# Performance work log

Measured on AMD Instinct MI355X. Metric: run time of the kernel, lower is better.

The kernel has to match this reference:

```python
import jax, jax.numpy as jnp
import numpy as np

KSIZE = 51  # radius=50 is even -> incremented to 51 in __init__


def _gaussian_1d(ksize):
    # cv2.getGaussianKernel with sigma<=0: sigma = 0.3*((ksize-1)*0.5 - 1) + 0.8
    sigma = 0.3 * ((ksize - 1) * 0.5 - 1) + 0.8
    x = np.arange(ksize, dtype=np.float64) - (ksize - 1) / 2
    g = np.exp(-(x * x) / (2.0 * sigma * sigma))
    g = g / g.sum()
    return g.astype(np.float32)


def _blur(img, kernel1d):
    """Separable Gaussian blur with reflect padding.
    Mathematically identical to the 2D conv with outer(g, g) in the torch code.
    img: (b, c, h, w), kernel1d: (k,)
    """
    k = kernel1d.shape[0]
    p = k // 2
    b, c, h, w = img.shape
    x = jnp.pad(img, ((0, 0), (0, 0), (p, p), (p, p)), mode='reflect')
    x = x.reshape(b * c, 1, h + 2 * p, w + 2 * p)
    # vertical pass then horizontal pass (conv vs correlation irrelevant: symmetric kernel)
    kv = kernel1d.reshape(1, 1, k, 1)
    kh = kernel1d.reshape(1, 1, 1, k)
    dn = ('NCHW', 'OIHW', 'NCHW')
    x = jax.lax.conv_general_dilated(x, kv, (1, 1), 'VALID', dimension_numbers=dn)
    x = jax.lax.conv_general_dilated(x, kh, (1, 1), 'VALID', dimension_numbers=dn)
    return x.reshape(b, c, h, w)


def setup_inputs() -> dict:
    key = jax.random.key(0)
    img = jax.random.uniform(key, (16, 3, 512, 512), dtype=jnp.float32)
    kernel1d = jnp.asarray(_gaussian_1d(KSIZE))
    return {"img": img, "kernel1d": kernel1d}


def reference(img, kernel1d):
    weight = 0.5
    threshold = 10.0
    blur = _blur(img, kernel1d)
    residual = img - blur
    mask = (jnp.abs(residual) * 255.0 > threshold).astype(img.dtype)
    soft_mask = _blur(mask, kernel1d)
    sharp = jnp.clip(img + weight * residual, 0.0, 1.0)
    return soft_mask * sharp + (1.0 - soft_mask) * img
```

## Files before the change

### kernel.cpp

```cpp
#include <hip/hip_runtime.h>
#include <hip/hip_bf16.h>


typedef __attribute__((ext_vector_type(8))) short bf16x8;
typedef __attribute__((ext_vector_type(4))) float f32x4;

constexpr int IMG = 512, NIMG = 48, K = 51;
constexpr int SP = 136;
constexpr int YP = 136;
constexpr int SROWS = 128;
constexpr int SDATA = 122;

__device__ __forceinline__ float bf2f(unsigned short u) {
    return __builtin_bit_cast(float, (unsigned)u << 16);
}
__device__ __forceinline__ unsigned short f2bf(float f) {
    unsigned u = __builtin_bit_cast(unsigned, f);
    u += 0x7FFF + ((u >> 16) & 1);
    return (unsigned short)(u >> 16);
}
__device__ __forceinline__ int refl(int i) {
    i = i < 0 ? -i : i;
    return i >= IMG ? 2 * IMG - 2 - i : i;
}

template <int PASS>
__global__ __launch_bounds__(512, 6) void usm_kern(const float* __restrict__ img,
                                                   unsigned short* __restrict__ resbuf,
                                                   unsigned char* __restrict__ maskbuf,
                                                   float* __restrict__ out,
                                                   const float* __restrict__ k1d) {
    __shared__ unsigned short st[SROWS * SP];
    __shared__ unsigned short Hl[64 * YP];

    const int tid = threadIdx.x, lane = tid & 63;
    const int wv = __builtin_amdgcn_readfirstlane(tid >> 6);
    const int m16 = lane & 15, g = lane >> 4;

    const int id = blockIdx.x;
    const int sw = (id & 7) * 384 + (id >> 3);
    const int bz = sw >> 6, r6 = sw & 63, byy = r6 >> 3, bxx = r6 & 7;
    const int x0 = bxx * 64, y0 = byy * 64;
    const size_t base = (size_t)bz * (IMG * IMG);
    const float* __restrict__ imgb = img + base;
    unsigned short* __restrict__ resb = resbuf + base;
    unsigned char* __restrict__ maskb = maskbuf + base;
    float* __restrict__ outb = out + base;

    bf16x8 a_v[2], a_h[2];
#pragma unroll
    for (int rs = 0; rs < 2; ++rs) {
        float gt[9];
#pragma unroll
        for (int e = 0; e < 9; ++e) {
            const int t = 32 * rs + 8 * g + e - m16;
            gt[e] = ((unsigned)t < (unsigned)K) ? k1d[t] : 0.f;
        }
#pragma unroll
        for (int j = 0; j < 8; ++j) {
            a_v[rs][j] = (short)f2bf(gt[j]);
            a_h[rs][j] = (short)f2bf(gt[j + 1]);
        }
    }
    const float gg0 = k1d[0], gg49 = k1d[49], gg50 = k1d[50];

    const bool xedge = (bxx == 0) | (bxx == 7);
    const int r0t = tid >> 4, c8 = (tid & 15) * 8;
#pragma unroll
    for (int j = 0; j < 4; ++j) {
        const int s = r0t + 32 * j;
        const int rowo = refl(y0 - 33 + min(s, SDATA - 1)) * IMG + (x0 - 32 + c8);
        unsigned pk[4];
        if (PASS == 0) {
            float v[8];
            if (!xedge) {
                const f32x4 f0 = *(const f32x4*)&imgb[rowo];
                const f32x4 f1 = *(const f32x4*)&imgb[rowo + 4];
#pragma unroll
                for (int e = 0; e < 4; ++e) { v[e] = f0[e]; v[e + 4] = f1[e]; }
            } else {
                const int rb = rowo - (x0 - 32 + c8);
#pragma unroll
                for (int e = 0; e < 8; ++e) v[e] = imgb[rb + refl(x0 - 32 + c8 + e)];
            }
#pragma unroll
            for (int w = 0; w < 4; ++w)
                pk[w] = (unsigned)f2bf(v[2 * w]) | ((unsigned)f2bf(v[2 * w + 1]) << 16);
        } else {
            unsigned char mb[8];
            if (!xedge) {
                const uint2 mv = *(const uint2*)&maskb[rowo];
#pragma unroll
                for (int e = 0; e < 4; ++e) {
                    mb[e] = (unsigned char)(mv.x >> (8 * e));
                    mb[e + 4] = (unsigned char)(mv.y >> (8 * e));
                }
            } else {
                const int rb = rowo - (x0 - 32 + c8);
#pragma unroll
                for (int e = 0; e < 8; ++e) mb[e] = maskb[rb + refl(x0 - 32 + c8 + e)];
            }
#pragma unroll
            for (int w = 0; w < 4; ++w)
                pk[w] = (mb[2 * w] ? 0x3F80u : 0u) | ((mb[2 * w + 1] ? 0x3F80u : 0u) << 16);
        }
        *(uint4*)&st[s * SP + c8] = make_uint4(pk[0], pk[1], pk[2], pk[3]);
    }
    __syncthreads();

#pragma unroll
    for (int k4 = 0; k4 < 4; ++k4) {
        const int t = wv + 8 * k4;
        const int xs = t & 3, yt = t >> 2;
        const int n = 16 * yt + m16;
        f32x4 acc = {0.f, 0.f, 0.f, 0.f};
#pragma unroll
        for (int rs = 0; rs < 2; ++rs) {
            const bf16x8 b = *(const bf16x8*)&st[n * SP + 16 * xs + 8 + 32 * rs + 8 * g];
            acc = __builtin_amdgcn_mfma_f32_16x16x32_bf16(a_h[rs], b, acc, 0, 0, 0);
        }
        if (g == 0) acc[0] = fmaf(gg0,  bf2f(st[n * SP + 16 * xs + 7]),  acc[0]);
        if (g == 3) acc[3] = fmaf(gg50, bf2f(st[n * SP + 16 * xs + 72]), acc[3]);
#pragma unroll
        for (int q = 0; q < 4; ++q)
            Hl[(16 * xs + 4 * g + q) * YP + n] = f2bf(acc[q]);
    }
    __syncthreads();

#pragma unroll
    for (int k2 = 0; k2 < 2; ++k2) {
        const int t = wv + 8 * k2;
        const int xs2 = t & 3, ys = t >> 2;
        const int xl = 16 * xs2 + m16;
        f32x4 acc = {0.f, 0.f, 0.f, 0.f};
#pragma unroll
        for (int rs = 0; rs < 2; ++rs) {
            const bf16x8 b = *(const bf16x8*)&Hl[xl * YP + 16 * ys + 8 + 32 * rs + 8 * g];
            acc = __builtin_amdgcn_mfma_f32_16x16x32_bf16(a_v[rs], b, acc, 0, 0, 0);
        }
        if (g == 3) {
            const float h72 = bf2f(Hl[xl * YP + 16 * ys + 72]);
            const float h73 = bf2f(Hl[xl * YP + 16 * ys + 73]);
            acc[2] = fmaf(gg50, h72, acc[2]);
            acc[3] = fmaf(gg49, h72, fmaf(gg50, h73, acc[3]));
        }
        const int yl0 = 16 * ys + 4 * g;
#pragma unroll
        for (int q = 0; q < 4; ++q) {
            const int di = (y0 + yl0 + q) * IMG + (x0 + xl);
            const float iv = imgb[di];
            if (PASS == 0) {
                const float rv = iv - acc[q];
                resb[di] = f2bf(rv);
                maskb[di] = (fabsf(rv) * 255.0f > 10.0f) ? 1 : 0;
            } else {
                const float rv = bf2f(resb[di]);
                float sharp = fmaf(0.5f, rv, iv);
                sharp = fminf(fmaxf(sharp, 0.f), 1.f);
                outb[di] = fmaf(acc[q], sharp - iv, iv);
            }
        }
    }
}

extern "C" void kernel_launch(void* const* d_in, const int* in_sizes, int n_in,
                              void* d_out, int out_size, void* d_ws, size_t ws_size,
                              hipStream_t stream) {
    (void)in_sizes; (void)n_in; (void)out_size; (void)ws_size;
    const float* img = (const float*)d_in[0];
    const float* k1d = (const float*)d_in[1];
    float* out = (float*)d_out;
    unsigned short* rs = (unsigned short*)d_ws;
    unsigned char* mk = (unsigned char*)d_ws + (size_t)NIMG * IMG * IMG * 2;

    const dim3 grid(NIMG * 64);

    usm_kern<0><<<grid, 512, 0, stream>>>(img, rs, mk, out, k1d);
    usm_kern<1><<<grid, 512, 0, stream>>>(img, rs, mk, out, k1d);
}
```

Before: 98.33 us.

## Swap MFMA operand roles for row-contiguous output and vectorized epilogue

Swaps the A/B operands of both MFMA passes so each lane's accumulator holds four consecutive x pixels. The intermediate LDS store then becomes a single 8-byte write, and the final global loads and stores become vector accesses (float4, uint2, uint32) instead of scalar strided ones. The image and residual loads for the epilogue are also prefetched before the first barrier to hide latency. The edge-tap corrections are reworked to fit the transposed output mapping, which adds more scalar LDS reads on the boundary lanes.

```diff
diff --git a/kernel.cpp b/kernel.cpp
--- a/kernel.cpp
+++ b/kernel.cpp
@@ -106,59 +106,93 @@
         }
         *(uint4*)&st[s * SP + c8] = make_uint4(pk[0], pk[1], pk[2], pk[3]);
     }
+
+    f32x4 ivp[2];
+    uint2 rvp[2];
+#pragma unroll
+    for (int k2 = 0; k2 < 2; ++k2) {
+        const int t = wv + 8 * k2;
+        const int xs = t & 3, ys = t >> 2;
+        const int di = (y0 + 16 * ys + m16) * IMG + (x0 + 16 * xs + 4 * g);
+        ivp[k2] = *(const f32x4*)&imgb[di];
+        if (PASS == 1) rvp[k2] = *(const uint2*)&resb[di];
+    }
     __syncthreads();
 
 #pragma unroll
     for (int k4 = 0; k4 < 4; ++k4) {
         const int t = wv + 8 * k4;
         const int xs = t & 3, yt = t >> 2;
-        const int n = 16 * yt + m16;
         f32x4 acc = {0.f, 0.f, 0.f, 0.f};
 #pragma unroll
         for (int rs = 0; rs < 2; ++rs) {
-            const bf16x8 b = *(const bf16x8*)&st[n * SP + 16 * xs + 8 + 32 * rs + 8 * g];
-            acc = __builtin_amdgcn_mfma_f32_16x16x32_bf16(a_h[rs], b, acc, 0, 0, 0);
-        }
-        if (g == 0) acc[0] = fmaf(gg0,  bf2f(st[n * SP + 16 * xs + 7]),  acc[0]);
-        if (g == 3) acc[3] = fmaf(gg50, bf2f(st[n * SP + 16 * xs + 72]), acc[3]);
-#pragma unroll
-        for (int q = 0; q < 4; ++q)
-            Hl[(16 * xs + 4 * g + q) * YP + n] = f2bf(acc[q]);
+            const bf16x8 ad = *(const bf16x8*)&st[(16 * yt + m16) * SP + 16 * xs + 8 + 32 * rs + 8 * g];
+            acc = __builtin_amdgcn_mfma_f32_16x16x32_bf16(ad, a_h[rs], acc, 0, 0, 0);
+        }
+        if (m16 == 0) {
+#pragma unroll
+            for (int q = 0; q < 4; ++q)
+                acc[q] = fmaf(gg0, bf2f(st[(16 * yt + 4 * g + q) * SP + 16 * xs + 7]), acc[q]);
+        }
+        if (m16 == 15) {
+#pragma unroll
+            for (int q = 0; q < 4; ++q)
+                acc[q] = fmaf(gg50, bf2f(st[(16 * yt + 4 * g + q) * SP + 16 * xs + 72]), acc[q]);
+        }
+        const unsigned lo = (unsigned)f2bf(acc[0]) | ((unsigned)f2bf(acc[1]) << 16);
+        const unsigned hi = (unsigned)f2bf(acc[2]) | ((unsigned)f2bf(acc[3]) << 16);
+        *(uint2*)&Hl[(16 * xs + m16) * YP + 16 * yt + 4 * g] = make_uint2(lo, hi);
     }
     __syncthreads();
 
 #pragma unroll
     for (int k2 = 0; k2 < 2; ++k2) {
         const int t = wv + 8 * k2;
-        const int xs2 = t & 3, ys = t >> 2;
-        const int xl = 16 * xs2 + m16;
+        const int xs = t & 3, ys = t >> 2;
         f32x4 acc = {0.f, 0.f, 0.f, 0.f};
 #pragma unroll
         for (int rs = 0; rs < 2; ++rs) {
-            const bf16x8 b = *(const bf16x8*)&Hl[xl * YP + 16 * ys + 8 + 32 * rs + 8 * g];
-            acc = __builtin_amdgcn_mfma_f32_16x16x32_bf16(a_v[rs], b, acc, 0, 0, 0);
-        }
-        if (g == 3) {
-            const float h72 = bf2f(Hl[xl * YP + 16 * ys + 72]);
-            const float h73 = bf2f(Hl[xl * YP + 16 * ys + 73]);
-            acc[2] = fmaf(gg50, h72, acc[2]);
-            acc[3] = fmaf(gg49, h72, fmaf(gg50, h73, acc[3]));
-        }
-        const int yl0 = 16 * ys + 4 * g;
-#pragma unroll
-        for (int q = 0; q < 4; ++q) {
-            const int di = (y0 + yl0 + q) * IMG + (x0 + xl);
-            const float iv = imgb[di];
-            if (PASS == 0) {
-                const float rv = iv - acc[q];
-                resb[di] = f2bf(rv);
-                maskb[di] = (fabsf(rv) * 255.0f > 10.0f) ? 1 : 0;
-            } else {
-                const float rv = bf2f(resb[di]);
-                float sharp = fmaf(0.5f, rv, iv);
+            const bf16x8 ah = *(const bf16x8*)&Hl[(16 * xs + m16) * YP + 16 * ys + 8 + 32 * rs + 8 * g];
+            acc = __builtin_amdgcn_mfma_f32_16x16x32_bf16(ah, a_v[rs], acc, 0, 0, 0);
+        }
+        if (m16 == 14) {
+#pragma unroll
+            for (int q = 0; q < 4; ++q)
+                acc[q] = fmaf(gg50, bf2f(Hl[(16 * xs + 4 * g + q) * YP + 16 * ys + 72]), acc[q]);
+        }
+        if (m16 == 15) {
+#pragma unroll
+            for (int q = 0; q < 4; ++q) {
+                const int hb = (16 * xs + 4 * g + q) * YP + 16 * ys;
+                acc[q] = fmaf(gg49, bf2f(Hl[hb + 72]), fmaf(gg50, bf2f(Hl[hb + 73]), acc[q]));
+            }
+        }
+        const int di = (y0 + 16 * ys + m16) * IMG + (x0 + 16 * xs + 4 * g);
+        const f32x4 iv = ivp[k2];
+        if (PASS == 0) {
+            unsigned mw = 0;
+            unsigned rp[2];
+            float rv[4];
+#pragma unroll
+            for (int q = 0; q < 4; ++q) {
+                rv[q] = iv[q] - acc[q];
+                mw |= (fabsf(rv[q]) * 255.0f > 10.0f ? 1u : 0u) << (8 * q);
+            }
+            rp[0] = (unsigned)f2bf(rv[0]) | ((unsigned)f2bf(rv[1]) << 16);
+            rp[1] = (unsigned)f2bf(rv[2]) | ((unsigned)f2bf(rv[3]) << 16);
+            *(uint2*)&resb[di] = make_uint2(rp[0], rp[1]);
+            *(unsigned*)&maskb[di] = mw;
+        } else {
+            f32x4 o;
+#pragma unroll
+            for (int q = 0; q < 4; ++q) {
+                const unsigned rw = (q < 2) ? rvp[k2].x : rvp[k2].y;
+                const float rvq = bf2f((unsigned short)(rw >> ((q & 1) * 16)));
+                float sharp = fmaf(0.5f, rvq, iv[q]);
                 sharp = fminf(fmaxf(sharp, 0.f), 1.f);
-                outb[di] = fmaf(acc[q], sharp - iv, iv);
-            }
+                o[q] = fmaf(acc[q], sharp - iv[q], iv[q]);
+            }
+            *(f32x4*)&outb[di] = o;
         }
     }
 }
```

Measured after the change: 113.1 us. +15.1%, slower.

## Stream four vertical tiles per block with rolling halo buffer; derive mask from residual

Applied to the files above, without the earlier changes.

Each block now processes a 64-wide by 256-tall column strip as four consecutive 64x64 tiles. A ring buffer in shared memory keeps the vertical halo rows, so only 64 new rows are loaded per tile, and the next tile's rows are prefetched while the current tile's blurs run. The separate byte mask buffer is removed: the second pass rebuilds the mask by thresholding the stored bf16 residual bits, which saves one global write and one read per pixel. In exchange, the grid has four times fewer blocks and each block runs a serial loop with extra barriers. The threshold is now applied to the bf16-rounded residual, which can flip the mask for values near the boundary.

```diff
diff --git a/kernel.cpp b/kernel.cpp
--- a/kernel.cpp
+++ b/kernel.cpp
@@ -8,7 +8,6 @@
 constexpr int IMG = 512, NIMG = 48, K = 51;
 constexpr int SP = 136;
 constexpr int YP = 136;
-constexpr int SROWS = 128;
 constexpr int SDATA = 122;
 
 __device__ __forceinline__ float bf2f(unsigned short u) {
@@ -27,10 +26,9 @@
 template <int PASS>
 __global__ __launch_bounds__(512, 6) void usm_kern(const float* __restrict__ img,
                                                    unsigned short* __restrict__ resbuf,
-                                                   unsigned char* __restrict__ maskbuf,
                                                    float* __restrict__ out,
                                                    const float* __restrict__ k1d) {
-    __shared__ unsigned short st[SROWS * SP];
+    __shared__ unsigned short st[128 * SP];
     __shared__ unsigned short Hl[64 * YP];
 
     const int tid = threadIdx.x, lane = tid & 63;
@@ -38,13 +36,12 @@
     const int m16 = lane & 15, g = lane >> 4;
 
     const int id = blockIdx.x;
-    const int sw = (id & 7) * 384 + (id >> 3);
-    const int bz = sw >> 6, r6 = sw & 63, byy = r6 >> 3, bxx = r6 & 7;
-    const int x0 = bxx * 64, y0 = byy * 64;
+    const int col = (id & 7) * 96 + (id >> 3);
+    const int bz = col >> 4, rr = col & 15, half = rr >> 3, bxx = rr & 7;
+    const int x0 = bxx * 64, ybase = half * 256;
     const size_t base = (size_t)bz * (IMG * IMG);
     const float* __restrict__ imgb = img + base;
     unsigned short* __restrict__ resb = resbuf + base;
-    unsigned char* __restrict__ maskb = maskbuf + base;
     float* __restrict__ outb = out + base;
 
     bf16x8 a_v[2], a_h[2];
@@ -65,101 +62,178 @@
     const float gg0 = k1d[0], gg49 = k1d[49], gg50 = k1d[50];
 
     const bool xedge = (bxx == 0) | (bxx == 7);
-    const int r0t = tid >> 4, c8 = (tid & 15) * 8;
-#pragma unroll
-    for (int j = 0; j < 4; ++j) {
-        const int s = r0t + 32 * j;
-        const int rowo = refl(y0 - 33 + min(s, SDATA - 1)) * IMG + (x0 - 32 + c8);
+    const int r0t = tid >> 4, c8 = (tid & 15) * 8, xoff = x0 - 32 + c8;
+
+#pragma unroll
+    for (int s4 = 0; s4 < 4; ++s4) {
+        const int s = r0t + 32 * s4;
+        const int rowb = refl(ybase - 33 + min(s, SDATA - 1)) * IMG;
         unsigned pk[4];
         if (PASS == 0) {
             float v[8];
             if (!xedge) {
-                const f32x4 f0 = *(const f32x4*)&imgb[rowo];
-                const f32x4 f1 = *(const f32x4*)&imgb[rowo + 4];
+                const f32x4 f0 = *(const f32x4*)&imgb[rowb + xoff];
+                const f32x4 f1 = *(const f32x4*)&imgb[rowb + xoff + 4];
 #pragma unroll
                 for (int e = 0; e < 4; ++e) { v[e] = f0[e]; v[e + 4] = f1[e]; }
             } else {
-                const int rb = rowo - (x0 - 32 + c8);
-#pragma unroll
-                for (int e = 0; e < 8; ++e) v[e] = imgb[rb + refl(x0 - 32 + c8 + e)];
+#pragma unroll
+                for (int e = 0; e < 8; ++e) v[e] = imgb[rowb + refl(xoff + e)];
             }
 #pragma unroll
             for (int w = 0; w < 4; ++w)
                 pk[w] = (unsigned)f2bf(v[2 * w]) | ((unsigned)f2bf(v[2 * w + 1]) << 16);
         } else {
-            unsigned char mb[8];
+            unsigned rw[4];
             if (!xedge) {
-                const uint2 mv = *(const uint2*)&maskb[rowo];
-#pragma unroll
-                for (int e = 0; e < 4; ++e) {
-                    mb[e] = (unsigned char)(mv.x >> (8 * e));
-                    mb[e + 4] = (unsigned char)(mv.y >> (8 * e));
-                }
-            } else {
-                const int rb = rowo - (x0 - 32 + c8);
-#pragma unroll
-                for (int e = 0; e < 8; ++e) mb[e] = maskb[rb + refl(x0 - 32 + c8 + e)];
-            }
-#pragma unroll
-            for (int w = 0; w < 4; ++w)
-                pk[w] = (mb[2 * w] ? 0x3F80u : 0u) | ((mb[2 * w + 1] ? 0x3F80u : 0u) << 16);
+                const uint4 q4 = *(const uint4*)&resb[rowb + xoff];
+                rw[0] = q4.x; rw[1] = q4.y; rw[2] = q4.z; rw[3] = q4.w;
+            } else {
+#pragma unroll
+                for (int w = 0; w < 4; ++w) {
+                    const unsigned short e0 = resb[rowb + refl(xoff + 2 * w)];
+                    const unsigned short e1 = resb[rowb + refl(xoff + 2 * w + 1)];
+                    rw[w] = (unsigned)e0 | ((unsigned)e1 << 16);
+                }
+            }
+#pragma unroll
+            for (int w = 0; w < 4; ++w) {
+                const unsigned lo = ((rw[w] & 0x7FFFu) > 0x3D20u) ? 0x3F80u : 0u;
+                const unsigned hi = (((rw[w] >> 16) & 0x7FFFu) > 0x3D20u) ? 0x3F80u : 0u;
+                pk[w] = lo | (hi << 16);
+            }
         }
         *(uint4*)&st[s * SP + c8] = make_uint4(pk[0], pk[1], pk[2], pk[3]);
     }
     __syncthreads();
 
-#pragma unroll
-    for (int k4 = 0; k4 < 4; ++k4) {
-        const int t = wv + 8 * k4;
-        const int xs = t & 3, yt = t >> 2;
-        const int n = 16 * yt + m16;
-        f32x4 acc = {0.f, 0.f, 0.f, 0.f};
-#pragma unroll
-        for (int rs = 0; rs < 2; ++rs) {
-            const bf16x8 b = *(const bf16x8*)&st[n * SP + 16 * xs + 8 + 32 * rs + 8 * g];
-            acc = __builtin_amdgcn_mfma_f32_16x16x32_bf16(a_h[rs], b, acc, 0, 0, 0);
-        }
-        if (g == 0) acc[0] = fmaf(gg0,  bf2f(st[n * SP + 16 * xs + 7]),  acc[0]);
-        if (g == 3) acc[3] = fmaf(gg50, bf2f(st[n * SP + 16 * xs + 72]), acc[3]);
-#pragma unroll
-        for (int q = 0; q < 4; ++q)
-            Hl[(16 * xs + 4 * g + q) * YP + n] = f2bf(acc[q]);
-    }
-    __syncthreads();
-
-#pragma unroll
-    for (int k2 = 0; k2 < 2; ++k2) {
-        const int t = wv + 8 * k2;
-        const int xs2 = t & 3, ys = t >> 2;
-        const int xl = 16 * xs2 + m16;
-        f32x4 acc = {0.f, 0.f, 0.f, 0.f};
-#pragma unroll
-        for (int rs = 0; rs < 2; ++rs) {
-            const bf16x8 b = *(const bf16x8*)&Hl[xl * YP + 16 * ys + 8 + 32 * rs + 8 * g];
-            acc = __builtin_amdgcn_mfma_f32_16x16x32_bf16(a_v[rs], b, acc, 0, 0, 0);
-        }
-        if (g == 3) {
-            const float h72 = bf2f(Hl[xl * YP + 16 * ys + 72]);
-            const float h73 = bf2f(Hl[xl * YP + 16 * ys + 73]);
-            acc[2] = fmaf(gg50, h72, acc[2]);
-            acc[3] = fmaf(gg49, h72, fmaf(gg50, h73, acc[3]));
-        }
-        const int yl0 = 16 * ys + 4 * g;
-#pragma unroll
-        for (int q = 0; q < 4; ++q) {
-            const int di = (y0 + yl0 + q) * IMG + (x0 + xl);
-            const float iv = imgb[di];
+#pragma unroll 1
+    for (int i = 0; i < 4; ++i) {
+        const int y0 = ybase + 64 * i;
+        const int off = (i & 1) << 6;
+
+        f32x4 nfa0, nfa1, nfb0, nfb1;
+        uint4 nma, nmb;
+        if (i < 3) {
+            const int y0n = y0 + 64;
+            const int rA = refl(y0n + 25 + r0t) * IMG;
+            const int rB = refl(y0n + 57 + r0t) * IMG;
             if (PASS == 0) {
-                const float rv = iv - acc[q];
-                resb[di] = f2bf(rv);
-                maskb[di] = (fabsf(rv) * 255.0f > 10.0f) ? 1 : 0;
-            } else {
-                const float rv = bf2f(resb[di]);
-                float sharp = fmaf(0.5f, rv, iv);
-                sharp = fminf(fmaxf(sharp, 0.f), 1.f);
-                outb[di] = fmaf(acc[q], sharp - iv, iv);
-            }
-        }
+                if (!xedge) {
+                    nfa0 = *(const f32x4*)&imgb[rA + xoff];
+                    nfa1 = *(const f32x4*)&imgb[rA + xoff + 4];
+                    nfb0 = *(const f32x4*)&imgb[rB + xoff];
+                    nfb1 = *(const f32x4*)&imgb[rB + xoff + 4];
+                } else {
+#pragma unroll
+                    for (int e = 0; e < 4; ++e) {
+                        nfa0[e] = imgb[rA + refl(xoff + e)];
+                        nfa1[e] = imgb[rA + refl(xoff + 4 + e)];
+                        nfb0[e] = imgb[rB + refl(xoff + e)];
+                        nfb1[e] = imgb[rB + refl(xoff + 4 + e)];
+                    }
+                }
+            } else {
+                if (!xedge) {
+                    nma = *(const uint4*)&resb[rA + xoff];
+                    nmb = *(const uint4*)&resb[rB + xoff];
+                } else {
+                    unsigned wa[4], wb[4];
+#pragma unroll
+                    for (int w = 0; w < 4; ++w) {
+                        wa[w] = (unsigned)resb[rA + refl(xoff + 2 * w)] |
+                                ((unsigned)resb[rA + refl(xoff + 2 * w + 1)] << 16);
+                        wb[w] = (unsigned)resb[rB + refl(xoff + 2 * w)] |
+                                ((unsigned)resb[rB + refl(xoff + 2 * w + 1)] << 16);
+                    }
+                    nma = make_uint4(wa[0], wa[1], wa[2], wa[3]);
+                    nmb = make_uint4(wb[0], wb[1], wb[2], wb[3]);
+                }
+            }
+        }
+
+#pragma unroll
+        for (int k4 = 0; k4 < 4; ++k4) {
+            const int t = wv + 8 * k4;
+            const int xs = t & 3, yt = t >> 2;
+            const int n = 16 * yt + m16;
+            const int sr = ((16 * yt + off) & 127) + m16;
+            f32x4 acc = {0.f, 0.f, 0.f, 0.f};
+#pragma unroll
+            for (int rs = 0; rs < 2; ++rs) {
+                const bf16x8 b = *(const bf16x8*)&st[sr * SP + 16 * xs + 8 + 32 * rs + 8 * g];
+                acc = __builtin_amdgcn_mfma_f32_16x16x32_bf16(a_h[rs], b, acc, 0, 0, 0);
+            }
+            if (g == 0) acc[0] = fmaf(gg0,  bf2f(st[sr * SP + 16 * xs + 7]),  acc[0]);
+            if (g == 3) acc[3] = fmaf(gg50, bf2f(st[sr * SP + 16 * xs + 72]), acc[3]);
+#pragma unroll
+            for (int q = 0; q < 4; ++q)
+                Hl[(16 * xs + 4 * g + q) * YP + n] = f2bf(acc[q]);
+        }
+        __syncthreads();
+
+        if (i < 3) {
+            const int noff = (~i & 1) << 6;
+            const int slA = ((58 + r0t + noff) & 127) * SP + c8;
+            const int slB = ((90 + r0t + noff) & 127) * SP + c8;
+            unsigned pa[4], pb[4];
+            if (PASS == 0) {
+                pa[0] = (unsigned)f2bf(nfa0[0]) | ((unsigned)f2bf(nfa0[1]) << 16);
+                pa[1] = (unsigned)f2bf(nfa0[2]) | ((unsigned)f2bf(nfa0[3]) << 16);
+                pa[2] = (unsigned)f2bf(nfa1[0]) | ((unsigned)f2bf(nfa1[1]) << 16);
+                pa[3] = (unsigned)f2bf(nfa1[2]) | ((unsigned)f2bf(nfa1[3]) << 16);
+                pb[0] = (unsigned)f2bf(nfb0[0]) | ((unsigned)f2bf(nfb0[1]) << 16);
+                pb[1] = (unsigned)f2bf(nfb0[2]) | ((unsigned)f2bf(nfb0[3]) << 16);
+                pb[2] = (unsigned)f2bf(nfb1[0]) | ((unsigned)f2bf(nfb1[1]) << 16);
+                pb[3] = (unsigned)f2bf(nfb1[2]) | ((unsigned)f2bf(nfb1[3]) << 16);
+            } else {
+                const unsigned wa[4] = {nma.x, nma.y, nma.z, nma.w};
+                const unsigned wb[4] = {nmb.x, nmb.y, nmb.z, nmb.w};
+#pragma unroll
+                for (int w = 0; w < 4; ++w) {
+                    pa[w] = (((wa[w] & 0x7FFFu) > 0x3D20u) ? 0x3F80u : 0u) |
+                            ((((wa[w] >> 16) & 0x7FFFu) > 0x3D20u) ? 0x3F800000u : 0u);
+                    pb[w] = (((wb[w] & 0x7FFFu) > 0x3D20u) ? 0x3F80u : 0u) |
+                            ((((wb[w] >> 16) & 0x7FFFu) > 0x3D20u) ? 0x3F800000u : 0u);
+                }
+            }
+            *(uint4*)&st[slA] = make_uint4(pa[0], pa[1], pa[2], pa[3]);
+            *(uint4*)&st[slB] = make_uint4(pb[0], pb[1], pb[2], pb[3]);
+        }
+
+#pragma unroll
+        for (int k2 = 0; k2 < 2; ++k2) {
+            const int t = wv + 8 * k2;
+            const int xs2 = t & 3, ys = t >> 2;
+            const int xl = 16 * xs2 + m16;
+            f32x4 acc = {0.f, 0.f, 0.f, 0.f};
+#pragma unroll
+            for (int rs = 0; rs < 2; ++rs) {
+                const bf16x8 b = *(const bf16x8*)&Hl[xl * YP + 16 * ys + 8 + 32 * rs + 8 * g];
+                acc = __builtin_amdgcn_mfma_f32_16x16x32_bf16(a_v[rs], b, acc, 0, 0, 0);
+            }
+            if (g == 3) {
+                const float h72 = bf2f(Hl[xl * YP + 16 * ys + 72]);
+                const float h73 = bf2f(Hl[xl * YP + 16 * ys + 73]);
+                acc[2] = fmaf(gg50, h72, acc[2]);
+                acc[3] = fmaf(gg49, h72, fmaf(gg50, h73, acc[3]));
+            }
+            const int yl0 = 16 * ys + 4 * g;
+#pragma unroll
+            for (int q = 0; q < 4; ++q) {
+                const int di = (y0 + yl0 + q) * IMG + (x0 + xl);
+                const float iv = imgb[di];
+                if (PASS == 0) {
+                    resb[di] = f2bf(iv - acc[q]);
+                } else {
+                    const float rv = bf2f(resb[di]);
+                    float sharp = fmaf(0.5f, rv, iv);
+                    sharp = fminf(fmaxf(sharp, 0.f), 1.f);
+                    outb[di] = fmaf(acc[q], sharp - iv, iv);
+                }
+            }
+        }
+        __syncthreads();
     }
 }
 
@@ -171,10 +245,9 @@
     const float* k1d = (const float*)d_in[1];
     float* out = (float*)d_out;
     unsigned short* rs = (unsigned short*)d_ws;
-    unsigned char* mk = (unsigned char*)d_ws + (size_t)NIMG * IMG * IMG * 2;
-
-    const dim3 grid(NIMG * 64);
-
-    usm_kern<0><<<grid, 512, 0, stream>>>(img, rs, mk, out, k1d);
-    usm_kern<1><<<grid, 512, 0, stream>>>(img, rs, mk, out, k1d);
-}
+
+    const dim3 grid(NIMG * 16);
+
+    usm_kern<0><<<grid, 512, 0, stream>>>(img, rs, out, k1d);
+    usm_kern<1><<<grid, 512, 0, stream>>>(img, rs, out, k1d);
+}
```

Result: slower. 100.6 us (+2.3%).
